# Performance work log

Hardware: AMD Instinct MI355X
Metric: run time of the kernel (lower is better)

## Reference

```python
import jax, jax.numpy as jnp
import numpy as np

EPS = 1e-12  # tf.math.l2_normalize epsilon

def _l2norm3(v):
    # 3 * l2_normalize(v, axis=-1), tf semantics: v / sqrt(max(sum(v^2), eps))
    sq = jnp.sum(v * v, axis=-1, keepdims=True)
    return 3.0 * v * jax.lax.rsqrt(jnp.maximum(sq, EPS))

def setup_inputs() -> dict:
    key = jax.random.key(0)
    k1, k2 = jax.random.split(key)
    B, C, D = 4096, 16384, 128
    inputs = jax.random.normal(k1, (B, D), dtype=jnp.float32)
    kernel = jax.random.normal(k2, (C, D), dtype=jnp.float32)
    return {"inputs": inputs, "kernel": kernel}

def reference(inputs, kernel):
    x = _l2norm3(inputs)        # [B, D]
    p = _l2norm3(kernel)        # [C, D]
    xs = jnp.sum(x * x, axis=-1, keepdims=True)          # [B, 1]
    ps = jnp.sum(p * p, axis=-1)                          # [C]
    cross = jnp.einsum('bd,cd->bc', x, p)                 # [B, C]
    return xs + ps[None, :] - 2.0 * cross                 # [B, C]
```

## Files before the change

kernel.cpp:

```cpp
#include <hip/hip_runtime.h>

typedef __attribute__((ext_vector_type(8))) short short8;
typedef __attribute__((ext_vector_type(4))) float f32x4;

__device__ __forceinline__ unsigned short f32_to_bf16(float f) {
    union { float f; unsigned int u; } c; c.f = f;
    unsigned int u = c.u;
    unsigned int r = (u + 0x7fffu + ((u >> 16) & 1u)) >> 16;
    return (unsigned short)r;
}

__global__ void norm_kernel(const float* __restrict__ in,
                            unsigned short* __restrict__ xout,
                            float* __restrict__ sout) {
    const int row  = blockIdx.x * 4 + (threadIdx.x >> 6);
    const int lane = threadIdx.x & 63;
    const float2 v = ((const float2*)(in + (size_t)row * 128))[lane];
    float s = fmaf(v.x, v.x, v.y * v.y);
#pragma unroll
    for (int off = 32; off; off >>= 1) s += __shfl_xor(s, off, 64);
    const float r  = rsqrtf(fmaxf(s, 1e-12f));
    const float sc = 3.0f * r;
    ushort2 o;
    o.x = f32_to_bf16(v.x * sc);
    o.y = f32_to_bf16(v.y * sc);
    ((ushort2*)(xout + (size_t)row * 128))[lane] = o;
    if (lane == 0) sout[row] = 9.0f * s * (r * r);
}

__global__ __launch_bounds__(256, 2) void gemm_kernel(
    const unsigned short* __restrict__ A,
    const unsigned short* __restrict__ B,
    const float* __restrict__ xs,
    const float* __restrict__ ps,
    float* __restrict__ out,
    int Ncols)
{
    __shared__ unsigned short sA[128 * 128];
    __shared__ unsigned short sB[128 * 128];

    const int tid  = threadIdx.x;
    const int lane = tid & 63;
    const int wave = tid >> 6;
    const int bm   = blockIdx.y;
    const int bn   = blockIdx.x;

    const int wm   = (wave >> 1) * 64;
    const int wn   = (wave & 1) * 64;
    const int l15  = lane & 15;
    const int quad = lane >> 4;

    float xsr[16];
    float psr[4];
#pragma unroll
    for (int mt = 0; mt < 4; ++mt)
#pragma unroll
        for (int r = 0; r < 4; ++r)
            xsr[mt * 4 + r] = xs[bm * 128 + wm + mt * 16 + quad * 4 + r];
#pragma unroll
    for (int nt = 0; nt < 4; ++nt)
        psr[nt] = ps[bn * 128 + wn + nt * 16 + l15];

    {
        const char* gA = (const char*)(A + (size_t)bm * 128 * 128);
        const char* gB = (const char*)(B + (size_t)bn * 128 * 128);
#pragma unroll
        for (int it = 0; it < 8; ++it) {
            const int cid = it * 256 + wave * 64 + lane;
            const int m   = cid >> 4;
            const int jj  = cid & 15;
            const int gj  = jj ^ (m & 7);
            const int gbyte = m * 256 + gj * 16;
            const int lbyte = cid * 16;
            __builtin_amdgcn_global_load_lds(
                (const __attribute__((address_space(1))) void*)(gA + gbyte),
                (__attribute__((address_space(3))) void*)((char*)sA + lbyte),
                16, 0, 0);
            __builtin_amdgcn_global_load_lds(
                (const __attribute__((address_space(1))) void*)(gB + gbyte),
                (__attribute__((address_space(3))) void*)((char*)sB + lbyte),
                16, 0, 0);
        }
    }
    __syncthreads();

    f32x4 acc[4][4];
#pragma unroll
    for (int i = 0; i < 4; ++i)
#pragma unroll
        for (int j = 0; j < 4; ++j)
            acc[i][j] = (f32x4){0.f, 0.f, 0.f, 0.f};

#pragma unroll
    for (int kk = 0; kk < 4; ++kk) {
        short8 af[4], bfv[4];
#pragma unroll
        for (int mt = 0; mt < 4; ++mt) {
            const int m  = wm + mt * 16 + l15;
            const int jj = (kk * 4 + quad) ^ (m & 7);
            af[mt] = *(const short8*)&sA[m * 128 + jj * 8];
        }
#pragma unroll
        for (int nt = 0; nt < 4; ++nt) {
            const int n  = wn + nt * 16 + l15;
            const int jj = (kk * 4 + quad) ^ (n & 7);
            bfv[nt] = *(const short8*)&sB[n * 128 + jj * 8];
        }
#pragma unroll
        for (int mt = 0; mt < 4; ++mt)
#pragma unroll
            for (int nt = 0; nt < 4; ++nt)
                acc[mt][nt] = __builtin_amdgcn_mfma_f32_16x16x32_bf16(
                    af[mt], bfv[nt], acc[mt][nt], 0, 0, 0);
    }

    const size_t stride = (size_t)Ncols;
#pragma unroll
    for (int mt = 0; mt < 4; ++mt) {
        const int rl   = wm + mt * 16 + quad * 4;
        const int grow = bm * 128 + rl;
#pragma unroll
        for (int nt = 0; nt < 4; ++nt) {
            const int gcol = bn * 128 + wn + nt * 16 + l15;
            const float pv = psr[nt];
            float* op = out + (size_t)grow * stride + gcol;
#pragma unroll
            for (int r = 0; r < 4; ++r) {
                op[(size_t)r * stride] =
                    fmaf(-2.0f, acc[mt][nt][r], xsr[mt * 4 + r] + pv);
            }
        }
    }
}

extern "C" void kernel_launch(void* const* d_in, const int* in_sizes, int n_in,
                              void* d_out, int out_size, void* d_ws, size_t ws_size,
                              hipStream_t stream) {
    const float* inputs = (const float*)d_in[0];
    const float* kern   = (const float*)d_in[1];
    float* out          = (float*)d_out;

    const int D = 128;
    const int B = in_sizes[0] / D;
    const int C = in_sizes[1] / D;

    char* ws = (char*)d_ws;
    unsigned short* xA = (unsigned short*)ws;
    unsigned short* pB = (unsigned short*)(ws + (size_t)B * D * 2);
    float* xs = (float*)(ws + (size_t)(B + C) * D * 2);
    float* ps = xs + B;

    norm_kernel<<<B / 4, 256, 0, stream>>>(inputs, xA, xs);
    norm_kernel<<<C / 4, 256, 0, stream>>>(kern, pB, ps);

    dim3 grid(C / 128, B / 128);
    gemm_kernel<<<grid, 256, 0, stream>>>(xA, pB, xs, ps, out, C);
}
```

Before: 278.6 us.

## Transpose MFMA operands for vectorized 16-byte output stores; merge norm launches

Swaps the A and B operands of the MFMA so each lane's four accumulator values run along the output columns rather than the rows. The epilogue can then write one float4 per tile instead of four scalar strided stores, and the row/column bias registers are remapped to match. Separately, the two normalization launches become a single launch that picks its source per row, which removes one kernel launch. The output write is the dominant cost of this GEMM (a 256 MB fp32 result), so store efficiency matters.

```diff
diff --git a/kernel.cpp b/kernel.cpp
--- a/kernel.cpp
+++ b/kernel.cpp
@@ -10,12 +10,16 @@
     return (unsigned short)r;
 }
 
-__global__ void norm_kernel(const float* __restrict__ in,
+__global__ void norm_kernel(const float* __restrict__ inA,
+                            const float* __restrict__ inB,
+                            int nA,
                             unsigned short* __restrict__ xout,
                             float* __restrict__ sout) {
     const int row  = blockIdx.x * 4 + (threadIdx.x >> 6);
     const int lane = threadIdx.x & 63;
-    const float2 v = ((const float2*)(in + (size_t)row * 128))[lane];
+    const float* src = (row < nA) ? (inA + (size_t)row * 128)
+                                  : (inB + (size_t)(row - nA) * 128);
+    const float2 v = ((const float2*)src)[lane];
     float s = fmaf(v.x, v.x, v.y * v.y);
 #pragma unroll
     for (int off = 32; off; off >>= 1) s += __shfl_xor(s, off, 64);
@@ -50,16 +54,16 @@
     const int l15  = lane & 15;
     const int quad = lane >> 4;
 
-    float xsr[16];
-    float psr[4];
+    float xsr[4];
+    float psr[16];
 #pragma unroll
     for (int mt = 0; mt < 4; ++mt)
+        xsr[mt] = xs[bm * 128 + wm + mt * 16 + l15];
+#pragma unroll
+    for (int nt = 0; nt < 4; ++nt)
 #pragma unroll
         for (int r = 0; r < 4; ++r)
-            xsr[mt * 4 + r] = xs[bm * 128 + wm + mt * 16 + quad * 4 + r];
-#pragma unroll
-    for (int nt = 0; nt < 4; ++nt)
-        psr[nt] = ps[bn * 128 + wn + nt * 16 + l15];
+            psr[nt * 4 + r] = ps[bn * 128 + wn + nt * 16 + quad * 4 + r];
 
     {
         const char* gA = (const char*)(A + (size_t)bm * 128 * 128);
@@ -111,24 +115,22 @@
 #pragma unroll
             for (int nt = 0; nt < 4; ++nt)
                 acc[mt][nt] = __builtin_amdgcn_mfma_f32_16x16x32_bf16(
-                    af[mt], bfv[nt], acc[mt][nt], 0, 0, 0);
+                    bfv[nt], af[mt], acc[mt][nt], 0, 0, 0);
     }
 
     const size_t stride = (size_t)Ncols;
 #pragma unroll
     for (int mt = 0; mt < 4; ++mt) {
-        const int rl   = wm + mt * 16 + quad * 4;
-        const int grow = bm * 128 + rl;
+        const int grow = bm * 128 + wm + mt * 16 + l15;
+        float* orow = out + (size_t)grow * stride;
 #pragma unroll
         for (int nt = 0; nt < 4; ++nt) {
-            const int gcol = bn * 128 + wn + nt * 16 + l15;
-            const float pv = psr[nt];
-            float* op = out + (size_t)grow * stride + gcol;
+            const int gcol = bn * 128 + wn + nt * 16 + quad * 4;
+            f32x4 v;
 #pragma unroll
-            for (int r = 0; r < 4; ++r) {
-                op[(size_t)r * stride] =
-                    fmaf(-2.0f, acc[mt][nt][r], xsr[mt * 4 + r] + pv);
-            }
+            for (int r = 0; r < 4; ++r)
+                v[r] = fmaf(-2.0f, acc[mt][nt][r], xsr[mt] + psr[nt * 4 + r]);
+            *(f32x4*)(orow + gcol) = v;
         }
     }
 }
@@ -150,8 +152,7 @@
     float* xs = (float*)(ws + (size_t)(B + C) * D * 2);
     float* ps = xs + B;
 
-    norm_kernel<<<B / 4, 256, 0, stream>>>(inputs, xA, xs);
-    norm_kernel<<<C / 4, 256, 0, stream>>>(kern, pB, ps);
+    norm_kernel<<<(B + C) / 4, 256, 0, stream>>>(inputs, kern, B, xA, xs);
 
     dim3 grid(C / 128, B / 128);
     gemm_kernel<<<grid, 256, 0, stream>>>(xA, pB, xs, ps, out, C);
```

Result: no change. 281.5 us (median of 2 runs) (+1.1%).
